# Optimization experiments

Measured on AMD Instinct MI355X. Metric: run time of the kernel, lower is better.

## Reference

```python
import jax, jax.numpy as jnp
import numpy as np

BN_EPS = 1e-5


def setup_inputs() -> dict:
    key = jax.random.key(0)
    ks = jax.random.split(key, 8)
    B, S, D = 2048, 64, 128      # batch, seq_len, d_in
    H, DK = 8, 16                # n_head, d_k; H*DK == 128
    F = H * DK
    std = np.sqrt(2.0 / DK).astype(np.float32)
    return {
        "v": jax.random.normal(ks[0], (B, S, D), jnp.float32),
        "Wq": jax.random.normal(ks[1], (F, D), jnp.float32) * std,
        "bq": jnp.zeros((F,), jnp.float32),
        "bn_gamma": jnp.ones((F,), jnp.float32),
        "bn_beta": jnp.zeros((F,), jnp.float32),
        "W2": jax.random.normal(ks[2], (F, F), jnp.float32) * (1.0 / np.sqrt(F)),
        "b2": jnp.zeros((F,), jnp.float32),
        "Wk": jax.random.normal(ks[3], (F, D), jnp.float32) * std,
        "bk": jnp.zeros((F,), jnp.float32),
    }


def reference(v, Wq, bq, bn_gamma, bn_beta, W2, b2, Wk, bk):
    # v: [B, S, D]
    B, S, D = v.shape
    F = Wq.shape[0]
    H = 8
    DK = F // H
    temperature = jnp.asarray(np.sqrt(DK), v.dtype)

    # q path: linear -> mean over seq -> BatchNorm1d (batch stats) -> linear
    q = jnp.einsum("bsd,fd->bsf", v, Wq) + bq          # [B, S, F]
    q = q.mean(axis=1)                                  # [B, F]
    mu = q.mean(axis=0)
    var = q.var(axis=0)                                 # biased, as BN uses
    q = (q - mu) * jax.lax.rsqrt(var + BN_EPS) * bn_gamma + bn_beta
    q = jnp.einsum("bf,gf->bg", q, W2) + b2             # [B, F]
    q = q.reshape(B, H, DK).transpose(1, 0, 2)          # [H, B, DK]

    # k path
    k = (jnp.einsum("bsd,fd->bsf", v, Wk) + bk).reshape(B, S, H, DK)
    k = k.transpose(2, 0, 1, 3)                         # [H, B, S, DK]

    # single query per (head, batch): scores over seq
    attn = jnp.einsum("hbd,hbsd->hbs", q, k) / temperature
    attn = jax.nn.softmax(attn, axis=-1)                # [H, B, S]
    # dropout is identity in eval mode

    # weighted sum over seq of the ORIGINAL v (torch repeats v per head;
    # broadcasting avoids materializing the repeat)
    out = jnp.einsum("hbs,bsd->hbd", attn, v)           # [H, B, D]
    return out, attn
```

## Files before the change

### kernel.cpp

```cpp
#include <hip/hip_runtime.h>

#define B_ 2048
#define S_ 64
#define D_ 128
#define F_ 128
#define H_ 8

__global__ __launch_bounds__(256) void k_q1(const float* __restrict__ v,
                                            const float* __restrict__ Wq,
                                            const float* __restrict__ bq,
                                            float* __restrict__ q1,
                                            float* __restrict__ gsum) {
  const int b = blockIdx.x;
  const int t = threadIdx.x;
  if (b == 0) gsum[t] = 0.f;

  __shared__ float red[8 * 128];
  __shared__ __align__(16) float vbarL[128];

  const int c4 = t & 31;
  const int r0 = t >> 5;
  const float4* v4 = (const float4*)(v + (size_t)b * (S_ * D_));
  float4 acc = {0.f, 0.f, 0.f, 0.f};
  #pragma unroll
  for (int i = 0; i < 8; ++i) {
    float4 x = v4[(r0 * 8 + i) * 32 + c4];
    acc.x += x.x; acc.y += x.y; acc.z += x.z; acc.w += x.w;
  }
  red[r0 * 128 + c4 * 4 + 0] = acc.x;
  red[r0 * 128 + c4 * 4 + 1] = acc.y;
  red[r0 * 128 + c4 * 4 + 2] = acc.z;
  red[r0 * 128 + c4 * 4 + 3] = acc.w;
  __syncthreads();
  if (t < 128) {
    float s = 0.f;
    #pragma unroll
    for (int r = 0; r < 8; ++r) s += red[r * 128 + t];
    vbarL[t] = s * (1.0f / 64.0f);
  }
  __syncthreads();

  const float4* Wq4 = (const float4*)Wq;
  const float4* vb4 = (const float4*)vbarL;
  const int d4 = t & 31;
  const int fg = t >> 5;
  #pragma unroll
  for (int fi = 0; fi < 16; ++fi) {
    int f = fi * 8 + fg;
    float4 w = Wq4[f * 32 + d4];
    float4 vv = vb4[d4];
    float p = w.x * vv.x + w.y * vv.y + w.z * vv.z + w.w * vv.w;
    #pragma unroll
    for (int off = 16; off; off >>= 1) p += __shfl_down(p, off, 32);
    if (d4 == 0) q1[b * F_ + f] = p + bq[f];
  }
}

__global__ __launch_bounds__(256) void k_stats2(const float* __restrict__ q1,
                                                const float* __restrict__ W2,
                                                float* __restrict__ gsum,
                                                float* __restrict__ gsq,
                                                float* __restrict__ W2t) {
  const int blk = blockIdx.x;
  const int t = threadIdx.x;
  const int f4 = t & 31, rg = t >> 5;
  const int r0 = blk * 32;
  const float4* q14 = (const float4*)q1;
  float4 s = {0.f, 0.f, 0.f, 0.f};
  float4 q = {0.f, 0.f, 0.f, 0.f};
  #pragma unroll
  for (int k = 0; k < 4; ++k) {
    float4 x = q14[(size_t)(r0 + rg + 8 * k) * 32 + f4];
    s.x += x.x; s.y += x.y; s.z += x.z; s.w += x.w;
    q.x += x.x * x.x; q.y += x.y * x.y; q.z += x.z * x.z; q.w += x.w * x.w;
  }
  __shared__ float rs[8][128], rq[8][128];
  rs[rg][f4 * 4 + 0] = s.x; rs[rg][f4 * 4 + 1] = s.y;
  rs[rg][f4 * 4 + 2] = s.z; rs[rg][f4 * 4 + 3] = s.w;
  rq[rg][f4 * 4 + 0] = q.x; rq[rg][f4 * 4 + 1] = q.y;
  rq[rg][f4 * 4 + 2] = q.z; rq[rg][f4 * 4 + 3] = q.w;
  __syncthreads();
  if (t < 128) {
    float ss = 0.f, qq = 0.f;
    #pragma unroll
    for (int r = 0; r < 8; ++r) { ss += rs[r][t]; qq += rq[r][t]; }
    atomicAdd(&gsum[t], ss);
    atomicAdd(&gsq[t], qq);
  }
  {
    int g = blk * 2 + (t >> 7);
    int f = t & 127;
    W2t[f * 128 + g] = W2[g * 128 + f];
  }
}

__global__ __launch_bounds__(256) void k_q2(const float* __restrict__ q1,
                                            const float* __restrict__ gsum,
                                            const float* __restrict__ gsq,
                                            const float* __restrict__ gamma,
                                            const float* __restrict__ beta,
                                            const float* __restrict__ W2t,
                                            const float* __restrict__ b2,
                                            float* __restrict__ q2) {
  const int b0 = blockIdx.x * 8;
  const int t = threadIdx.x;
  __shared__ float scaleL[128], shiftL[128];
  __shared__ __align__(16) float qnL[8 * 128];

  if (t < 128) {
    float mu = gsum[t] * (1.0f / (float)B_);
    float var = gsq[t] * (1.0f / (float)B_) - mu * mu;
    float rsg = rsqrtf(var + 1e-5f) * gamma[t];
    scaleL[t] = rsg;
    shiftL[t] = beta[t] - mu * rsg;
  }
  __syncthreads();
  {
    int row = t >> 5, f4 = t & 31;
    float4 x = ((const float4*)q1)[(size_t)(b0 + row) * 32 + f4];
    x.x = x.x * scaleL[f4 * 4 + 0] + shiftL[f4 * 4 + 0];
    x.y = x.y * scaleL[f4 * 4 + 1] + shiftL[f4 * 4 + 1];
    x.z = x.z * scaleL[f4 * 4 + 2] + shiftL[f4 * 4 + 2];
    x.w = x.w * scaleL[f4 * 4 + 3] + shiftL[f4 * 4 + 3];
    ((float4*)qnL)[row * 32 + f4] = x;
  }
  __syncthreads();

  const int r = t >> 5, g4 = t & 31;
  const float4* W2t4 = (const float4*)W2t;
  float4 acc = ((const float4*)b2)[g4];
  #pragma unroll 8
  for (int f = 0; f < 128; ++f) {
    float4 w = W2t4[f * 32 + g4];
    float qv = qnL[r * 128 + f];
    acc.x += qv * w.x; acc.y += qv * w.y; acc.z += qv * w.z; acc.w += qv * w.w;
  }
  ((float4*)q2)[(size_t)(b0 + r) * 32 + g4] = acc;
}

__global__ __launch_bounds__(256) void k_attn(const float* __restrict__ v,
                                              const float* __restrict__ q2,
                                              const float* __restrict__ Wk,
                                              const float* __restrict__ bk,
                                              float* __restrict__ outp) {
  const int b = blockIdx.x;
  const int t = threadIdx.x;
  __shared__ __align__(16) float vL[64 * 128];
  __shared__ __align__(16) float qWL[8 * 128];
  __shared__ __align__(16) float q2L[128];
  __shared__ float attnL[8 * 64];
  __shared__ float qbL[8];

  float4* vL4 = (float4*)vL;
  const float4* vg4 = (const float4*)(v + (size_t)b * (S_ * D_));
  #pragma unroll
  for (int i = 0; i < 8; ++i) {
    int idx = i * 256 + t;
    int s = idx >> 5, c4 = idx & 31;
    vL4[s * 32 + (c4 ^ (s & 31))] = vg4[idx];
  }
  if (t < 32) ((float4*)q2L)[t] = ((const float4*)q2)[(size_t)b * 32 + t];
  __syncthreads();

  {
    const int h = t >> 5, d4 = t & 31;
    const float4* Wk4 = (const float4*)Wk;
    const float* q2row = &q2L[h * 16];
    float4 acc = {0.f, 0.f, 0.f, 0.f};
    #pragma unroll
    for (int dk = 0; dk < 16; ++dk) {
      float qv = q2row[dk];
      float4 w = Wk4[(h * 16 + dk) * 32 + d4];
      acc.x += qv * w.x; acc.y += qv * w.y; acc.z += qv * w.z; acc.w += qv * w.w;
    }
    ((float4*)qWL)[h * 32 + d4] = acc;
  }
  if (t < 8) {
    float acc = 0.f;
    #pragma unroll
    for (int dk = 0; dk < 16; ++dk)
      acc += q2L[t * 16 + dk] * bk[t * 16 + dk];
    qbL[t] = acc;
  }
  __syncthreads();

  const int s = t & 63;
  const int hq = t >> 6;
  const int h0 = hq * 2, h1 = hq * 2 + 1;
  const float4* qWL4 = (const float4*)qWL;
  float a0 = 0.f, a1 = 0.f;
  #pragma unroll
  for (int d4 = 0; d4 < 32; ++d4) {
    float4 vv = vL4[s * 32 + (d4 ^ (s & 31))];
    float4 w0 = qWL4[h0 * 32 + d4];
    float4 w1 = qWL4[h1 * 32 + d4];
    a0 += vv.x * w0.x + vv.y * w0.y + vv.z * w0.z + vv.w * w0.w;
    a1 += vv.x * w1.x + vv.y * w1.y + vv.z * w1.z + vv.w * w1.w;
  }
  float l0 = (a0 + qbL[h0]) * 0.25f;
  float l1 = (a1 + qbL[h1]) * 0.25f;

  float m0 = l0, m1 = l1;
  #pragma unroll
  for (int off = 32; off; off >>= 1) {
    m0 = fmaxf(m0, __shfl_xor(m0, off, 64));
    m1 = fmaxf(m1, __shfl_xor(m1, off, 64));
  }
  float e0 = __expf(l0 - m0), e1 = __expf(l1 - m1);
  float s0 = e0, s1 = e1;
  #pragma unroll
  for (int off = 32; off; off >>= 1) {
    s0 += __shfl_xor(s0, off, 64);
    s1 += __shfl_xor(s1, off, 64);
  }
  float at0 = e0 / s0, at1 = e1 / s1;
  attnL[h0 * 64 + s] = at0;
  attnL[h1 * 64 + s] = at1;
  float* attn_out = outp + (size_t)H_ * B_ * D_;
  attn_out[(size_t)h0 * (B_ * S_) + b * S_ + s] = at0;
  attn_out[(size_t)h1 * (B_ * S_) + b * S_ + s] = at1;
  __syncthreads();

  const int d4o = t & 31;
  const int h = t >> 5;
  float4 acc = {0.f, 0.f, 0.f, 0.f};
  #pragma unroll
  for (int si = 0; si < 64; ++si) {
    float a = attnL[h * 64 + si];
    float4 vv = vL4[si * 32 + (d4o ^ (si & 31))];
    acc.x += a * vv.x; acc.y += a * vv.y; acc.z += a * vv.z; acc.w += a * vv.w;
  }
  ((float4*)outp)[(size_t)h * (B_ * 32) + b * 32 + d4o] = acc;
}

extern "C" void kernel_launch(void* const* d_in, const int* in_sizes, int n_in,
                              void* d_out, int out_size, void* d_ws, size_t ws_size,
                              hipStream_t stream) {
  const float* v     = (const float*)d_in[0];
  const float* Wq    = (const float*)d_in[1];
  const float* bq    = (const float*)d_in[2];
  const float* gamma = (const float*)d_in[3];
  const float* beta  = (const float*)d_in[4];
  const float* W2    = (const float*)d_in[5];
  const float* b2    = (const float*)d_in[6];
  const float* Wk    = (const float*)d_in[7];
  const float* bk    = (const float*)d_in[8];

  float* ws = (float*)d_ws;
  float* q1v  = ws;
  float* q2v  = q1v + (size_t)B_ * F_;
  float* gsum = q2v + (size_t)B_ * F_;
  float* gsq  = gsum + 128;
  float* W2t  = gsq + 128;
  float* outp = (float*)d_out;

  hipLaunchKernelGGL(k_q1,     dim3(B_),  dim3(256), 0, stream, v, Wq, bq, q1v, gsum);
  hipLaunchKernelGGL(k_stats2, dim3(64),  dim3(256), 0, stream, q1v, W2, gsum, gsq, W2t);
  hipLaunchKernelGGL(k_q2,     dim3(256), dim3(256), 0, stream, q1v, gsum, gsq, gamma, beta, W2t, b2, q2v);
  hipLaunchKernelGGL(k_attn,   dim3(B_),  dim3(256), 0, stream, v, q2v, Wk, bk, outp);
}
```

Measured before the change: 59.98 us.

## Fuse BatchNorm and second linear layer into the attention kernel

Removes the separate k_q2 kernel and the W2 transpose. Each attention block now applies BatchNorm to its own q1 row and computes its q2 row itself as a 128x128 matvec against untransposed W2, using pairs of threads and a shuffle reduction. This saves one kernel launch and the q2 round trip through global memory. In exchange, every attention block reads all of W2 (64KB, mostly from cache) and adds an extra barrier before the attention work.

```diff
diff --git a/kernel.cpp b/kernel.cpp
--- a/kernel.cpp
+++ b/kernel.cpp
@@ -57,10 +57,8 @@
 }
 
 __global__ __launch_bounds__(256) void k_stats2(const float* __restrict__ q1,
-                                                const float* __restrict__ W2,
                                                 float* __restrict__ gsum,
-                                                float* __restrict__ gsq,
-                                                float* __restrict__ W2t) {
+                                                float* __restrict__ gsq) {
   const int blk = blockIdx.x;
   const int t = threadIdx.x;
   const int f4 = t & 31, rg = t >> 5;
@@ -87,59 +85,16 @@
     atomicAdd(&gsum[t], ss);
     atomicAdd(&gsq[t], qq);
   }
-  {
-    int g = blk * 2 + (t >> 7);
-    int f = t & 127;
-    W2t[f * 128 + g] = W2[g * 128 + f];
-  }
-}
-
-__global__ __launch_bounds__(256) void k_q2(const float* __restrict__ q1,
-                                            const float* __restrict__ gsum,
-                                            const float* __restrict__ gsq,
-                                            const float* __restrict__ gamma,
-                                            const float* __restrict__ beta,
-                                            const float* __restrict__ W2t,
-                                            const float* __restrict__ b2,
-                                            float* __restrict__ q2) {
-  const int b0 = blockIdx.x * 8;
-  const int t = threadIdx.x;
-  __shared__ float scaleL[128], shiftL[128];
-  __shared__ __align__(16) float qnL[8 * 128];
-
-  if (t < 128) {
-    float mu = gsum[t] * (1.0f / (float)B_);
-    float var = gsq[t] * (1.0f / (float)B_) - mu * mu;
-    float rsg = rsqrtf(var + 1e-5f) * gamma[t];
-    scaleL[t] = rsg;
-    shiftL[t] = beta[t] - mu * rsg;
-  }
-  __syncthreads();
-  {
-    int row = t >> 5, f4 = t & 31;
-    float4 x = ((const float4*)q1)[(size_t)(b0 + row) * 32 + f4];
-    x.x = x.x * scaleL[f4 * 4 + 0] + shiftL[f4 * 4 + 0];
-    x.y = x.y * scaleL[f4 * 4 + 1] + shiftL[f4 * 4 + 1];
-    x.z = x.z * scaleL[f4 * 4 + 2] + shiftL[f4 * 4 + 2];
-    x.w = x.w * scaleL[f4 * 4 + 3] + shiftL[f4 * 4 + 3];
-    ((float4*)qnL)[row * 32 + f4] = x;
-  }
-  __syncthreads();
-
-  const int r = t >> 5, g4 = t & 31;
-  const float4* W2t4 = (const float4*)W2t;
-  float4 acc = ((const float4*)b2)[g4];
-  #pragma unroll 8
-  for (int f = 0; f < 128; ++f) {
-    float4 w = W2t4[f * 32 + g4];
-    float qv = qnL[r * 128 + f];
-    acc.x += qv * w.x; acc.y += qv * w.y; acc.z += qv * w.z; acc.w += qv * w.w;
-  }
-  ((float4*)q2)[(size_t)(b0 + r) * 32 + g4] = acc;
 }
 
 __global__ __launch_bounds__(256) void k_attn(const float* __restrict__ v,
-                                              const float* __restrict__ q2,
+                                              const float* __restrict__ q1,
+                                              const float* __restrict__ gsum,
+                                              const float* __restrict__ gsq,
+                                              const float* __restrict__ gamma,
+                                              const float* __restrict__ beta,
+                                              const float* __restrict__ W2,
+                                              const float* __restrict__ b2,
                                               const float* __restrict__ Wk,
                                               const float* __restrict__ bk,
                                               float* __restrict__ outp) {
@@ -147,6 +102,7 @@
   const int t = threadIdx.x;
   __shared__ __align__(16) float vL[64 * 128];
   __shared__ __align__(16) float qWL[8 * 128];
+  __shared__ __align__(16) float qnL[128];
   __shared__ __align__(16) float q2L[128];
   __shared__ float attnL[8 * 64];
   __shared__ float qbL[8];
@@ -159,7 +115,29 @@
     int s = idx >> 5, c4 = idx & 31;
     vL4[s * 32 + (c4 ^ (s & 31))] = vg4[idx];
   }
-  if (t < 32) ((float4*)q2L)[t] = ((const float4*)q2)[(size_t)b * 32 + t];
+
+  if (t < 128) {
+    float mu = gsum[t] * (1.0f / (float)B_);
+    float var = gsq[t] * (1.0f / (float)B_) - mu * mu;
+    float rsg = rsqrtf(var + 1e-5f) * gamma[t];
+    qnL[t] = q1[(size_t)b * F_ + t] * rsg + (beta[t] - mu * rsg);
+  }
+  __syncthreads();
+
+  {
+    const int g = t >> 1, hf = t & 1;
+    const float4* W24 = (const float4*)W2;
+    const float4* qn4 = (const float4*)qnL;
+    float p = 0.f;
+    #pragma unroll
+    for (int k = 0; k < 16; ++k) {
+      float4 w = W24[g * 32 + hf * 16 + k];
+      float4 qv = qn4[hf * 16 + k];
+      p += w.x * qv.x + w.y * qv.y + w.z * qv.z + w.w * qv.w;
+    }
+    p += __shfl_xor(p, 1, 64);
+    if (hf == 0) q2L[g] = p + b2[g];
+  }
   __syncthreads();
 
   {
@@ -248,14 +226,12 @@
 
   float* ws = (float*)d_ws;
   float* q1v  = ws;
-  float* q2v  = q1v + (size_t)B_ * F_;
-  float* gsum = q2v + (size_t)B_ * F_;
+  float* gsum = q1v + (size_t)B_ * F_;
   float* gsq  = gsum + 128;
-  float* W2t  = gsq + 128;
   float* outp = (float*)d_out;
 
-  hipLaunchKernelGGL(k_q1,     dim3(B_),  dim3(256), 0, stream, v, Wq, bq, q1v, gsum);
-  hipLaunchKernelGGL(k_stats2, dim3(64),  dim3(256), 0, stream, q1v, W2, gsum, gsq, W2t);
-  hipLaunchKernelGGL(k_q2,     dim3(256), dim3(256), 0, stream, q1v, gsum, gsq, gamma, beta, W2t, b2, q2v);
-  hipLaunchKernelGGL(k_attn,   dim3(B_),  dim3(256), 0, stream, v, q2v, Wk, bk, outp);
-}
+  hipLaunchKernelGGL(k_q1,     dim3(B_), dim3(256), 0, stream, v, Wq, bq, q1v, gsum);
+  hipLaunchKernelGGL(k_stats2, dim3(64), dim3(256), 0, stream, q1v, gsum, gsq);
+  hipLaunchKernelGGL(k_attn,   dim3(B_), dim3(256), 0, stream, v, q1v, gsum, gsq,
+                     gamma, beta, W2, b2, Wk, bk, outp);
+}
```

Result: slower. 61.51 us (+2.5%).

## Move q·Wk projection into q2 kernel and pass qW to attention

Applied to the files above, without the earlier changes.

The per-batch projection of q2 through Wk (qW) and the bias term qb now run in the k_q2 kernel, 8 batches per block, and are written to workspace. The attention kernel just loads the precomputed qW row and qb values, which removes a dependent Wk projection phase and one sync from its prologue. The cost is extra global traffic: qW is 4KB per batch written and then read back, versus the 512B q2 row read before.

```diff
diff --git a/kernel.cpp b/kernel.cpp
--- a/kernel.cpp
+++ b/kernel.cpp
@@ -94,18 +94,22 @@
   }
 }
 
-__global__ __launch_bounds__(256) void k_q2(const float* __restrict__ q1,
-                                            const float* __restrict__ gsum,
-                                            const float* __restrict__ gsq,
-                                            const float* __restrict__ gamma,
-                                            const float* __restrict__ beta,
-                                            const float* __restrict__ W2t,
-                                            const float* __restrict__ b2,
-                                            float* __restrict__ q2) {
+__global__ __launch_bounds__(256) void k_q2qw(const float* __restrict__ q1,
+                                              const float* __restrict__ gsum,
+                                              const float* __restrict__ gsq,
+                                              const float* __restrict__ gamma,
+                                              const float* __restrict__ beta,
+                                              const float* __restrict__ W2t,
+                                              const float* __restrict__ b2,
+                                              const float* __restrict__ Wk,
+                                              const float* __restrict__ bk,
+                                              float* __restrict__ qW,
+                                              float* __restrict__ qb) {
   const int b0 = blockIdx.x * 8;
   const int t = threadIdx.x;
   __shared__ float scaleL[128], shiftL[128];
   __shared__ __align__(16) float qnL[8 * 128];
+  __shared__ __align__(16) float q2L[8 * 128];
 
   if (t < 128) {
     float mu = gsum[t] * (1.0f / (float)B_);
@@ -126,62 +130,69 @@
   }
   __syncthreads();
 
-  const int r = t >> 5, g4 = t & 31;
-  const float4* W2t4 = (const float4*)W2t;
-  float4 acc = ((const float4*)b2)[g4];
-  #pragma unroll 8
-  for (int f = 0; f < 128; ++f) {
-    float4 w = W2t4[f * 32 + g4];
-    float qv = qnL[r * 128 + f];
-    acc.x += qv * w.x; acc.y += qv * w.y; acc.z += qv * w.z; acc.w += qv * w.w;
-  }
-  ((float4*)q2)[(size_t)(b0 + r) * 32 + g4] = acc;
-}
-
-__global__ __launch_bounds__(256) void k_attn(const float* __restrict__ v,
-                                              const float* __restrict__ q2,
-                                              const float* __restrict__ Wk,
-                                              const float* __restrict__ bk,
-                                              float* __restrict__ outp) {
-  const int b = blockIdx.x;
-  const int t = threadIdx.x;
-  __shared__ __align__(16) float vL[64 * 128];
-  __shared__ __align__(16) float qWL[8 * 128];
-  __shared__ __align__(16) float q2L[128];
-  __shared__ float attnL[8 * 64];
-  __shared__ float qbL[8];
-
-  float4* vL4 = (float4*)vL;
-  const float4* vg4 = (const float4*)(v + (size_t)b * (S_ * D_));
+  {
+    const int r = t >> 5, g4 = t & 31;
+    const float4* W2t4 = (const float4*)W2t;
+    float4 acc = ((const float4*)b2)[g4];
+    #pragma unroll 8
+    for (int f = 0; f < 128; ++f) {
+      float4 w = W2t4[f * 32 + g4];
+      float qv = qnL[r * 128 + f];
+      acc.x += qv * w.x; acc.y += qv * w.y; acc.z += qv * w.z; acc.w += qv * w.w;
+    }
+    ((float4*)q2L)[r * 32 + g4] = acc;
+  }
+  __syncthreads();
+
+  const float4* Wk4 = (const float4*)Wk;
   #pragma unroll
   for (int i = 0; i < 8; ++i) {
-    int idx = i * 256 + t;
-    int s = idx >> 5, c4 = idx & 31;
-    vL4[s * 32 + (c4 ^ (s & 31))] = vg4[idx];
-  }
-  if (t < 32) ((float4*)q2L)[t] = ((const float4*)q2)[(size_t)b * 32 + t];
-  __syncthreads();
-
-  {
-    const int h = t >> 5, d4 = t & 31;
-    const float4* Wk4 = (const float4*)Wk;
-    const float* q2row = &q2L[h * 16];
+    int o4 = i * 256 + t;
+    int bi = o4 >> 8, h = (o4 >> 5) & 7, d4 = o4 & 31;
     float4 acc = {0.f, 0.f, 0.f, 0.f};
+    const float* q2row = &q2L[bi * 128 + h * 16];
     #pragma unroll
     for (int dk = 0; dk < 16; ++dk) {
       float qv = q2row[dk];
       float4 w = Wk4[(h * 16 + dk) * 32 + d4];
       acc.x += qv * w.x; acc.y += qv * w.y; acc.z += qv * w.z; acc.w += qv * w.w;
     }
-    ((float4*)qWL)[h * 32 + d4] = acc;
-  }
-  if (t < 8) {
+    ((float4*)qW)[(size_t)(b0 + bi) * 256 + h * 32 + d4] = acc;
+  }
+  if (t < 64) {
+    int bi = t >> 3, h = t & 7;
     float acc = 0.f;
     #pragma unroll
     for (int dk = 0; dk < 16; ++dk)
-      acc += q2L[t * 16 + dk] * bk[t * 16 + dk];
-    qbL[t] = acc;
-  }
+      acc += q2L[bi * 128 + h * 16 + dk] * bk[h * 16 + dk];
+    qb[(b0 + bi) * 8 + h] = acc;
+  }
+}
+
+__global__ __launch_bounds__(256) void k_attn(const float* __restrict__ v,
+                                              const float* __restrict__ qW,
+                                              const float* __restrict__ qb,
+                                              float* __restrict__ outp) {
+  const int b = blockIdx.x;
+  const int t = threadIdx.x;
+  __shared__ __align__(16) float vL[64 * 128];
+  __shared__ __align__(16) float qWL[8 * 128];
+  __shared__ float attnL[8 * 64];
+  __shared__ float qbL[8];
+
+  float4* vL4 = (float4*)vL;
+  const float4* vg4 = (const float4*)(v + (size_t)b * (S_ * D_));
+  #pragma unroll
+  for (int i = 0; i < 8; ++i) {
+    int idx = i * 256 + t;
+    int s = idx >> 5, c4 = idx & 31;
+    vL4[s * 32 + (c4 ^ (s & 31))] = vg4[idx];
+  }
+  {
+    const float4* qWg4 = (const float4*)(qW + (size_t)b * (H_ * D_));
+    ((float4*)qWL)[t] = qWg4[t];
+  }
+  if (t < 8) qbL[t] = qb[b * 8 + t];
   __syncthreads();
 
   const int s = t & 63;
@@ -248,14 +259,16 @@
 
   float* ws = (float*)d_ws;
   float* q1v  = ws;
-  float* q2v  = q1v + (size_t)B_ * F_;
-  float* gsum = q2v + (size_t)B_ * F_;
+  float* gsum = q1v + (size_t)B_ * F_;
   float* gsq  = gsum + 128;
   float* W2t  = gsq + 128;
+  float* qWv  = W2t + 128 * 128;
+  float* qbv  = qWv + (size_t)B_ * H_ * D_;
   float* outp = (float*)d_out;
 
   hipLaunchKernelGGL(k_q1,     dim3(B_),  dim3(256), 0, stream, v, Wq, bq, q1v, gsum);
   hipLaunchKernelGGL(k_stats2, dim3(64),  dim3(256), 0, stream, q1v, W2, gsum, gsq, W2t);
-  hipLaunchKernelGGL(k_q2,     dim3(256), dim3(256), 0, stream, q1v, gsum, gsq, gamma, beta, W2t, b2, q2v);
-  hipLaunchKernelGGL(k_attn,   dim3(B_),  dim3(256), 0, stream, v, q2v, Wk, bk, outp);
-}
+  hipLaunchKernelGGL(k_q2qw,   dim3(256), dim3(256), 0, stream, q1v, gsum, gsq,
+                     gamma, beta, W2t, b2, Wk, bk, qWv, qbv);
+  hipLaunchKernelGGL(k_attn,   dim3(B_),  dim3(256), 0, stream, v, qWv, qbv, outp);
+}
```

Result: slower. 71.38 us (+19.0%).
